# Kernel tuning notes

Hardware: AMD Instinct MI355X
Metric: run time of the kernel (lower is better)

Reference implementation:

```python
import jax, jax.numpy as jnp
import numpy as np

SEG_NUMS = [1, 2, 4, 8, 16, 32, 64, 128, 256, 512]
L = SEG_NUMS[-1]
B, C, VOCAB = 32, 64, 8192
BETA = 0.25
RESI = 0.5  # quant_resi_ratio
N_PHI = 4
# PhiPartiallyShared ticks for K==4: linspace(1/(3K), 1-1/(3K), K)
PHI_TICKS = np.linspace(1.0 / (3 * N_PHI), 1.0 - 1.0 / (3 * N_PHI), N_PHI)


def interp_area(x, size):
    """torch F.interpolate(mode='area') for [B,C,l] when sizes divide evenly."""
    b, c, l = x.shape
    if size == l:
        return x
    if size < l:  # adaptive avg pool == block mean (l % size == 0)
        return x.reshape(b, c, size, l // size).mean(axis=-1)
    return jnp.repeat(x, size // l, axis=-1)  # area upsample == repeat


def phi_apply(h, w, b):
    """Phi: h*(1-r) + Conv1d(h)*r, same padding, ks=3. h:[B,C,l] w:[C,C,3] b:[C]."""
    y = jax.lax.conv_general_dilated(h, w, window_strides=(1,), padding=[(1, 1)],
                                     dimension_numbers=('NCH', 'OIH', 'NCH'))
    y = y + b[None, :, None]
    return h * (1.0 - RESI) + y * RESI


def _normalize(x, axis):
    return x / jnp.maximum(jnp.linalg.norm(x, axis=axis, keepdims=True), 1e-12)


def _mse(a, b):
    return jnp.mean((a - b) ** 2)


def setup_inputs() -> dict:
    key = jax.random.key(0)
    k1, k2, k3 = jax.random.split(key, 3)
    f_BCl = jax.random.normal(k1, (B, C, L), jnp.float32)
    embed_w = jax.random.normal(k2, (VOCAB, C), jnp.float32)
    phi_w = jax.random.normal(k3, (N_PHI, C, C, 3), jnp.float32) * 0.05  # conv-init scale
    phi_b = jnp.zeros((N_PHI, C), jnp.float32)
    return {"f_BCl": f_BCl, "embed_w": embed_w, "phi_w": phi_w, "phi_b": phi_b}


def vq_forward(f, embed_w, phi_w, phi_b):
    f = f.astype(jnp.float32)
    f_ng = jax.lax.stop_gradient(f)
    f_rest = f_ng
    f_hat = jnp.zeros_like(f_ng)
    loss = jnp.asarray(0.0, jnp.float32)
    # argmax uses .data (stop-grad) normalized codebook columns
    cb_n = _normalize(jax.lax.stop_gradient(embed_w), axis=1)  # [V, C]
    num_scales = len(SEG_NUMS)
    for si, s in enumerate(SEG_NUMS):
        rest = interp_area(f_rest, s)                      # [B, C, s] (identity at last scale)
        rest_NC = _normalize(rest.transpose(0, 2, 1).reshape(-1, C), axis=1)  # [B*s, C]
        idx = jnp.argmax(rest_NC @ cb_n.T, axis=1)         # [B*s] cosine-sim lookup
        h = embed_w[idx].reshape(B, s, C).transpose(0, 2, 1)  # gather (differentiable) -> [B,C,s]
        h = interp_area(h, L)
        pidx = int(np.argmin(np.abs(PHI_TICKS - si / (num_scales - 1))))
        h = phi_apply(h, phi_w[pidx], phi_b[pidx])
        f_hat = f_hat + h
        f_rest = f_rest - h
        loss = loss + BETA * _mse(jax.lax.stop_gradient(f_hat), f) + _mse(f_hat, f_ng)
    loss = loss / num_scales
    f_hat_out = jax.lax.stop_gradient(f_hat) - f_ng + f  # straight-through
    return f_hat_out, loss


def reference(f_BCl, embed_w, phi_w, phi_b):
    return vq_forward(f_BCl, embed_w, phi_w, phi_b)
```

## Files before the change

kernel.cpp:

```cpp
#include <hip/hip_runtime.h>


#define B_ 32
#define C_ 64
#define L_ 512
#define V_ 8192

typedef _Float16 half8 __attribute__((ext_vector_type(8)));
typedef float f32x4 __attribute__((ext_vector_type(4)));

#define C11 4.8828125e-4f

__device__ __forceinline__ unsigned enc_f(float s) {
  unsigned u = __float_as_uint(s);
  return (u & 0x80000000u) ? ~u : (u | 0x80000000u);
}

__device__ __forceinline__ void split2(float x, _Float16& h, _Float16& m) {
  h = (_Float16)x;
  float r1 = x - (float)h;
  m = (_Float16)(r1 * 2048.0f);
}

__global__ __launch_bounds__(256) void k_setup(
    const float* __restrict__ f, const float* __restrict__ embed,
    const float* __restrict__ phiw, _Float16* __restrict__ ch,
    _Float16* __restrict__ cm, float* __restrict__ restAll,
    float* __restrict__ lossac, unsigned long long* __restrict__ packed,
    float* __restrict__ phiwT) {
  const int blk = blockIdx.x;
  const int tid = threadIdx.x;
  if (blk < 128) {
    int g = blk * 256 + tid;
    int v = g >> 2;
    int sub = g & 3;
    const float* row = embed + v * 64 + sub * 16;
    float x[16];
    float ss = 0.f;
#pragma unroll
    for (int i = 0; i < 16; i += 4) {
      float4 t = *(const float4*)(row + i);
      x[i] = t.x; x[i + 1] = t.y; x[i + 2] = t.z; x[i + 3] = t.w;
      ss += t.x * t.x + t.y * t.y + t.z * t.z + t.w * t.w;
    }
    ss += __shfl_xor(ss, 1);
    ss += __shfl_xor(ss, 2);
    float rinv = 1.0f / fmaxf(sqrtf(ss), 1e-12f);
    _Float16 hb[16], mb[16];
#pragma unroll
    for (int i = 0; i < 16; i++) split2(x[i] * rinv, hb[i], mb[i]);
    const int kc = sub >> 1;
    const int q0 = (2 * sub) & 3;
    const int q1 = (2 * sub + 1) & 3;
    const int m = v & 15;
    const int blkbase = ((v >> 4) * 2 + kc) * 512;
    *(half8*)(ch + blkbase + (q0 * 16 + m) * 8) = *(half8*)(hb);
    *(half8*)(ch + blkbase + (q1 * 16 + m) * 8) = *(half8*)(hb + 8);
    *(half8*)(cm + blkbase + (q0 * 16 + m) * 8) = *(half8*)(mb);
    *(half8*)(cm + blkbase + (q1 * 16 + m) * 8) = *(half8*)(mb + 8);
  } else if (blk < 640) {
    int sb = blk - 128;
    int b = sb >> 4;
    int c = (sb & 15) * 4 + (tid >> 6);
    int lane = tid & 63;
    const float* row = f + (b * 64 + c) * 512 + lane * 8;
    float4 x0 = *(const float4*)row;
    float4 x1 = *(const float4*)(row + 4);
    float ssum = ((x0.x + x0.y) + (x0.z + x0.w)) +
                 ((x1.x + x1.y) + (x1.z + x1.w));
#pragma unroll
    for (int off = 32; off > 0; off >>= 1) ssum += __shfl_down(ssum, off);
    if (lane == 0) restAll[c * 32 + b] = ssum;
  } else {
    int zg = (blk - 640) * 256 + tid;
    const int ZS = 512 * 256;
    for (int i = zg; i < 126976; i += ZS) restAll[2048 + i] = 0.0f;
    for (int i = zg; i < 32736; i += ZS) packed[i] = 0ull;
    if (zg < 5120) lossac[zg] = 0.0f;
    if (phiwT) {
      for (int i = zg; i < 49152; i += ZS) {
        float v = phiw[i];
        int p = i / 12288;
        int r = i - p * 12288;
        int o = r / 192;
        int r2 = r - o * 192;
        int c = r2 / 3;
        int t = r2 - c * 3;
        phiwT[((p * 3 + t) * 64 + c) * 64 + o] = v;
      }
    }
  }
}

#define ARG_LOAD(BH0, BH1, BM0, BM1, TT)                                   \
  {                                                                        \
    const _Float16* p1 = ch + (code_start + (TT)) * 64 + lane * 8;         \
    const _Float16* p2 = cm + (code_start + (TT)) * 64 + lane * 8;         \
    BH0 = *(const half8*)(p1);                                             \
    BH1 = *(const half8*)(p1 + 512);                                       \
    BM0 = *(const half8*)(p2);                                             \
    BM1 = *(const half8*)(p2 + 512);                                       \
  }

#define ARG_TILE(BH0, BH1, BM0, BM1, TT)                                   \
  {                                                                        \
    const int cid = cs_g + (TT) + m;                                       \
    _Pragma("unroll") for (int mt = 0; mt < MT; mt++) {                    \
      f32x4 a0, a1;                                                        \
      a0 = __builtin_amdgcn_mfma_f32_16x16x32_f16(ah[mt][0], BH0, Z, 0, 0, 0); \
      a1 = __builtin_amdgcn_mfma_f32_16x16x32_f16(ah[mt][0], BM0, Z, 0, 0, 0); \
      a1 = __builtin_amdgcn_mfma_f32_16x16x32_f16(am[mt][0], BH0, a1, 0, 0, 0); \
      a0 = __builtin_amdgcn_mfma_f32_16x16x32_f16(ah[mt][1], BH1, a0, 0, 0, 0); \
      a1 = __builtin_amdgcn_mfma_f32_16x16x32_f16(ah[mt][1], BM1, a1, 0, 0, 0); \
      a1 = __builtin_amdgcn_mfma_f32_16x16x32_f16(am[mt][1], BH1, a1, 0, 0, 0); \
      _Pragma("unroll") for (int r = 0; r < 4; r++) {                      \
        float sc = fmaf(C11, a1[r], a0[r]);                                \
        if (sc > best[mt][r]) { best[mt][r] = sc; bidx[mt][r] = cid; }     \
      }                                                                    \
    }                                                                      \
  }

template <int MT>
__global__ __launch_bounds__(256, 2) void k_argmax3(
    const _Float16* __restrict__ ch, const _Float16* __restrict__ cm,
    const float* __restrict__ restq, unsigned long long* __restrict__ packedq,
    int Q, int mgroups, int wave_codes, int cbase) {
  const int mg = blockIdx.x % mgroups;
  const int sp = blockIdx.x / mgroups;
  const int lane = threadIdx.x & 63;
  const int wave = threadIdx.x >> 6;
  const int qbase = mg * (MT * 16);
  __shared__ _Float16 qh[MT * 16][72];
  __shared__ _Float16 qm[MT * 16][72];
  __shared__ unsigned long long spart[4][MT * 16];
  for (int i = threadIdx.x; i < MT * 16 * 64; i += 256) {
    int c = i / (MT * 16);
    int qq = i % (MT * 16);
    float v = restq[c * Q + qbase + qq];
    _Float16 h, m;
    split2(v, h, m);
    qh[qq][c] = h;
    qm[qq][c] = m;
  }
  __syncthreads();

  const int m = lane & 15;
  const int quad = lane >> 4;
  half8 ah[MT][2], am[MT][2];
#pragma unroll
  for (int mt = 0; mt < MT; mt++)
#pragma unroll
    for (int kc = 0; kc < 2; kc++) {
      ah[mt][kc] = *(const half8*)(&qh[mt * 16 + m][kc * 32 + quad * 8]);
      am[mt][kc] = *(const half8*)(&qm[mt * 16 + m][kc * 32 + quad * 8]);
    }

  float best[MT][4];
  int bidx[MT][4];
#pragma unroll
  for (int mt = 0; mt < MT; mt++)
#pragma unroll
    for (int r = 0; r < 4; r++) { best[mt][r] = -3.4e38f; bidx[mt][r] = 0; }

  const int code_start = (sp * 4 + wave) * wave_codes;
  const int cs_g = cbase + code_start;
  const f32x4 Z = {0.f, 0.f, 0.f, 0.f};

  half8 Ah0, Ah1, Am0, Am1, Bh0, Bh1, Bm0, Bm1;
  ARG_LOAD(Ah0, Ah1, Am0, Am1, 0);
  if (16 < wave_codes) ARG_LOAD(Bh0, Bh1, Bm0, Bm1, 16);
  for (int t = 0; t < wave_codes; t += 32) {
    ARG_TILE(Ah0, Ah1, Am0, Am1, t);
    if (t + 32 < wave_codes) ARG_LOAD(Ah0, Ah1, Am0, Am1, t + 32);
    if (t + 16 < wave_codes) {
      ARG_TILE(Bh0, Bh1, Bm0, Bm1, t + 16);
      if (t + 48 < wave_codes) ARG_LOAD(Bh0, Bh1, Bm0, Bm1, t + 48);
    }
  }

#pragma unroll
  for (int off = 1; off < 16; off <<= 1) {
#pragma unroll
    for (int mt = 0; mt < MT; mt++)
#pragma unroll
      for (int r = 0; r < 4; r++) {
        float ob = __shfl_xor(best[mt][r], off);
        int oi = __shfl_xor(bidx[mt][r], off);
        if (ob > best[mt][r] || (ob == best[mt][r] && oi < bidx[mt][r])) {
          best[mt][r] = ob; bidx[mt][r] = oi;
        }
      }
  }
  if (m == 0) {
#pragma unroll
    for (int mt = 0; mt < MT; mt++)
#pragma unroll
      for (int r = 0; r < 4; r++) {
        unsigned long long pk =
            ((unsigned long long)enc_f(best[mt][r]) << 32) |
            (unsigned)(~bidx[mt][r]);
        spart[wave][mt * 16 + quad * 4 + r] = pk;
      }
  }
  __syncthreads();
  if (threadIdx.x < MT * 16) {
    unsigned long long v = spart[0][threadIdx.x];
    unsigned long long v1 = spart[1][threadIdx.x];
    unsigned long long v2 = spart[2][threadIdx.x];
    unsigned long long v3 = spart[3][threadIdx.x];
    if (v1 > v) v = v1;
    if (v2 > v) v = v2;
    if (v3 > v) v = v3;
    atomicMax(&packedq[qbase + threadIdx.x], v);
  }
}

__global__ __launch_bounds__(256) void k_fused(
    const float* __restrict__ f, const float* __restrict__ embed,
    const float* __restrict__ phiw, const float* __restrict__ phib,
    const float* __restrict__ wT, const unsigned long long* __restrict__ packedq,
    float* __restrict__ restn, float* __restrict__ fhat,
    float* __restrict__ lossac, int s, int log2blk, int pidx, int si,
    int log2blkn) {
  const int ch0 = blockIdx.x * 32;
  const int bb = blockIdx.y;
  const int tid = threadIdx.x;
  const int blkw = 1 << log2blk;
  int j_lo = (ch0 >> log2blk) - 1;
  if (j_lo < 0) j_lo = 0;
  int j_hi = ((ch0 + 31) >> log2blk) + 1;
  if (j_hi > s - 1) j_hi = s - 1;
  const int nseg = j_hi - j_lo + 1;

  __shared__ float hl[34][64];
  __shared__ float abc_l[34][192];

  for (int i = tid; i < nseg * 64; i += 256) {
    int seg = i >> 6, c = i & 63;
    int idx = (int)(~(unsigned)(packedq[bb * s + j_lo + seg]));
    hl[seg][c] = embed[idx * 64 + c];
  }
  __syncthreads();

  {
    const int o = tid & 63;
    const int w4 = tid >> 6;
    const float* wrow = phiw + (pidx * 64 + o) * 192;
    const float* wtp = wT ? (wT + pidx * 12288 + o) : nullptr;
    float acc[9][3];
#pragma unroll
    for (int a = 0; a < 9; a++) { acc[a][0] = acc[a][1] = acc[a][2] = 0.f; }
#pragma unroll
    for (int c4b = 0; c4b < 4; c4b++) {
      float w48[48];
      if (wT) {
        const float* wp = wtp + c4b * 16 * 64;
#pragma unroll
        for (int cc = 0; cc < 16; cc++)
#pragma unroll
          for (int k = 0; k < 3; k++)
            w48[cc * 3 + k] = wp[(k * 64 + cc) * 64];
      } else {
#pragma unroll
        for (int k = 0; k < 12; k++)
          *(float4*)(w48 + 4 * k) = *(const float4*)(wrow + c4b * 48 + 4 * k);
      }
#pragma unroll
      for (int sx = 0; sx < 9; sx++) {
        int seg = w4 + sx * 4;
        if (seg < nseg) {
#pragma unroll
          for (int cc4 = 0; cc4 < 4; cc4++) {
            float4 h4 = *(const float4*)(&hl[seg][c4b * 16 + cc4 * 4]);
            const float hv[4] = {h4.x, h4.y, h4.z, h4.w};
#pragma unroll
            for (int u = 0; u < 4; u++) {
              int cc = cc4 * 4 + u;
              acc[sx][0] = fmaf(w48[cc * 3 + 0], hv[u], acc[sx][0]);
              acc[sx][1] = fmaf(w48[cc * 3 + 1], hv[u], acc[sx][1]);
              acc[sx][2] = fmaf(w48[cc * 3 + 2], hv[u], acc[sx][2]);
            }
          }
        }
      }
    }
#pragma unroll
    for (int sx = 0; sx < 9; sx++) {
      int seg = w4 + sx * 4;
      if (seg < nseg) {
        abc_l[seg][o] = acc[sx][0];
        abc_l[seg][64 + o] = acc[sx][1];
        abc_l[seg][128 + o] = acc[sx][2];
      }
    }
  }
  __syncthreads();

  const int c = tid >> 2;
  const int l0 = ch0 + (tid & 3) * 8;
  const float bias = phib[pidx * 64 + c];
  const int fi0 = (bb * 64 + c) * 512 + l0;
  const float4 fa = *(const float4*)(f + fi0);
  const float4 fb2 = *(const float4*)(f + fi0 + 4);
  float fv[8] = {fa.x, fa.y, fa.z, fa.w, fb2.x, fb2.y, fb2.z, fb2.w};
  float fhv[8] = {0.f, 0.f, 0.f, 0.f, 0.f, 0.f, 0.f, 0.f};
  if (si != 0) {
    const float4 ga = *(const float4*)(fhat + fi0);
    const float4 gb2 = *(const float4*)(fhat + fi0 + 4);
    fhv[0] = ga.x; fhv[1] = ga.y; fhv[2] = ga.z; fhv[3] = ga.w;
    fhv[4] = gb2.x; fhv[5] = gb2.y; fhv[6] = gb2.z; fhv[7] = gb2.w;
  }
  float dv[8];
  float sq = 0.f;
#pragma unroll
  for (int k = 0; k < 8; k++) {
    int l = l0 + k;
    int j = l >> log2blk;
    int jrel = j - j_lo;
    int pos = l & (blkw - 1);
    float y = abc_l[jrel][64 + c] + bias;
    if (pos == 0) {
      if (j > 0) y += abc_l[jrel - 1][c];
    } else {
      y += abc_l[jrel][c];
    }
    if (pos == blkw - 1) {
      if (j < s - 1) y += abc_l[jrel + 1][128 + c];
    } else {
      y += abc_l[jrel][128 + c];
    }
    float ho = 0.5f * (hl[jrel][c] + y);
    float fh = fhv[k] + ho;
    fhv[k] = fh;
    float d = fh - fv[k];
    dv[k] = d;
    sq = fmaf(d, d, sq);
  }
  *(float4*)(fhat + fi0) = make_float4(fhv[0], fhv[1], fhv[2], fhv[3]);
  *(float4*)(fhat + fi0 + 4) = make_float4(fhv[4], fhv[5], fhv[6], fhv[7]);

  if (log2blkn >= 0) {
    const int sn = 512 >> log2blkn;
    const int blkn = 1 << log2blkn;
    const int qb = c * (32 * sn) + bb * sn;
    float rs8 = -(((dv[0] + dv[1]) + (dv[2] + dv[3])) +
                  ((dv[4] + dv[5]) + (dv[6] + dv[7])));
    if (blkn >= 64) {
      float r = rs8;
      r += __shfl_down(r, 2);
      r += __shfl_down(r, 1);
      if ((tid & 3) == 0) atomicAdd(&restn[qb + (l0 >> log2blkn)], r);
    } else if (blkn == 32) {
      float r = rs8;
      r += __shfl_down(r, 2);
      r += __shfl_down(r, 1);
      if ((tid & 3) == 0) restn[qb + (l0 >> 5)] = r;
    } else if (blkn == 16) {
      float r = rs8;
      r += __shfl_down(r, 1);
      if ((tid & 1) == 0) restn[qb + (l0 >> 4)] = r;
    } else if (blkn == 8) {
      restn[qb + (l0 >> 3)] = rs8;
    } else {
      for (int base = 0; base < 8; base += blkn) {
        float rs = 0.f;
        for (int k = 0; k < blkn; k++) rs += dv[base + k];
        restn[qb + ((l0 + base) >> log2blkn)] = -rs;
      }
    }
  }

#pragma unroll
  for (int off = 32; off > 0; off >>= 1) sq += __shfl_down(sq, off);
  __shared__ float red[4];
  const int lane = tid & 63, wave = tid >> 6;
  if (lane == 0) red[wave] = sq;
  __syncthreads();
  if (tid == 0)
    lossac[si * 512 + bb * 16 + blockIdx.x] =
        (red[0] + red[1]) + (red[2] + red[3]);
}

__global__ __launch_bounds__(256) void k_loss(const float* __restrict__ lossac,
                                              float* __restrict__ out) {
  const int tid = threadIdx.x;
  float sum = 0.f;
  for (int i = tid; i < 5120; i += 256) sum += lossac[i];
#pragma unroll
  for (int off = 32; off > 0; off >>= 1) sum += __shfl_down(sum, off);
  __shared__ float red[4];
  if ((tid & 63) == 0) red[tid >> 6] = sum;
  __syncthreads();
  if (tid == 0)
    out[B_ * C_ * L_] = ((red[0] + red[1]) + (red[2] + red[3])) *
                        (1.25f / (10.0f * (float)(B_ * C_ * L_)));
}

extern "C" void kernel_launch(void* const* d_in, const int* in_sizes, int n_in,
                              void* d_out, int out_size, void* d_ws,
                              size_t ws_size, hipStream_t stream) {
  const float* f     = (const float*)d_in[0];
  const float* embed = (const float*)d_in[1];
  const float* phiw  = (const float*)d_in[2];
  const float* phib  = (const float*)d_in[3];
  float* fhat = (float*)d_out;

  _Float16* ch = (_Float16*)d_ws;
  _Float16* cm = ch + V_ * 64;
  float* restAll = (float*)(cm + V_ * 64);
  float* lossac = restAll + 2048 * 1023;
  unsigned long long* packed = (unsigned long long*)(lossac + 5120);
  float* phiwT = (float*)(packed + 32736);
  const size_t WS_NEED = (size_t)((char*)(phiwT + 49152) - (char*)d_ws);
  if (ws_size < WS_NEED) phiwT = nullptr;

  static const int PIDX[10] = {0, 0, 1, 1, 1, 2, 2, 3, 3, 3};
  static const int NSPL[10] = {16, 16, 16, 16, 16, 16, 16, 16, 8, 4};

  k_setup<<<dim3(1152), dim3(256), 0, stream>>>(f, embed, phiw, ch, cm,
                                                restAll, lossac, packed,
                                                phiwT);

  for (int si = 0; si < 10; si++) {
    const int s = 1 << si;
    const int Q = 32 * s;
    const int log2blk = 9 - si;
    const int nsplit = NSPL[si];
    const int wave_codes = V_ / nsplit / 4;
    const float* restq = restAll + 2048 * (s - 1);
    unsigned long long* pq = packed + 32 * (s - 1);

    if (Q >= 64) {
      const int mgroups = Q / 64;
      k_argmax3<4><<<dim3(mgroups * nsplit), dim3(256), 0, stream>>>(
          ch, cm, restq, pq, Q, mgroups, wave_codes, 0);
    } else {
      k_argmax3<2><<<dim3(nsplit), dim3(256), 0, stream>>>(
          ch, cm, restq, pq, Q, 1, wave_codes, 0);
    }

    float* restn = (si < 9) ? (restAll + 2048 * (2 * s - 1)) : nullptr;
    const int log2blkn = (si < 9) ? (8 - si) : -1;
    k_fused<<<dim3(16, 32), dim3(256), 0, stream>>>(
        f, embed, phiw, phib, phiwT, pq, restn, fhat, lossac, s, log2blk,
        PIDX[si], si, log2blkn);
  }
  k_loss<<<dim3(1), dim3(256), 0, stream>>>(lossac, fhat);
}
```

Before: 516.7 us.

## Fuse all stages into one persistent kernel with software grid barriers

Replaces the setup kernel, the twenty per-scale argmax/fused launches and the loss kernel with a single persistent 512-block kernel. Stages are separated by an atomic-counter grid barrier with flag polling, and shared memory is reused through a union. The aim is to remove launch overhead and inter-kernel gaps across about 22 small launches. In exchange, all 512 blocks must be co-resident or the barrier deadlocks, and barrier latency plus idle blocks in the small argmax stages add cost. The phiwT fallback for an undersized workspace is also dropped.

```diff
diff --git a/kernel.cpp b/kernel.cpp
--- a/kernel.cpp
+++ b/kernel.cpp
@@ -5,11 +5,25 @@
 #define C_ 64
 #define L_ 512
 #define V_ 8192
+#define NBLK 512
 
 typedef _Float16 half8 __attribute__((ext_vector_type(8)));
 typedef float f32x4 __attribute__((ext_vector_type(4)));
 
 #define C11 4.8828125e-4f
+
+union SMem {
+  struct {
+    _Float16 qh[64][72];
+    _Float16 qm[64][72];
+    unsigned long long spart[4][64];
+  } am;
+  struct {
+    float hl[34][64];
+    float abc[34][192];
+    float red[4];
+  } fu;
+};
 
 __device__ __forceinline__ unsigned enc_f(float s) {
   unsigned u = __float_as_uint(s);
@@ -22,13 +36,33 @@
   m = (_Float16)(r1 * 2048.0f);
 }
 
-__global__ __launch_bounds__(256) void k_setup(
-    const float* __restrict__ f, const float* __restrict__ embed,
-    const float* __restrict__ phiw, _Float16* __restrict__ ch,
-    _Float16* __restrict__ cm, float* __restrict__ restAll,
-    float* __restrict__ lossac, unsigned long long* __restrict__ packed,
-    float* __restrict__ phiwT) {
-  const int blk = blockIdx.x;
+__device__ __forceinline__ void gbar(unsigned long long* gb, unsigned bar) {
+  __syncthreads();
+  if (threadIdx.x == 0) {
+    __threadfence();
+    unsigned long long old = atomicAdd(gb, 1ull);
+    if (old == (unsigned long long)bar * NBLK - 1ull) {
+#pragma unroll
+      for (int i = 0; i < 8; i++)
+        atomicExch(gb + 32 + i * 32, (unsigned long long)bar);
+    } else {
+      unsigned long long* myf = gb + 32 + (blockIdx.x & 7) * 32;
+      while (atomicAdd(myf, 0ull) < (unsigned long long)bar)
+        __builtin_amdgcn_s_sleep(16);
+    }
+    __threadfence();
+  }
+  __syncthreads();
+}
+
+__device__ void d_setup(int blk, const float* __restrict__ f,
+                        const float* __restrict__ embed,
+                        const float* __restrict__ phiw,
+                        _Float16* __restrict__ ch, _Float16* __restrict__ cm,
+                        float* __restrict__ restAll,
+                        float* __restrict__ lossac,
+                        unsigned long long* __restrict__ packed,
+                        float* __restrict__ phiwT) {
   const int tid = threadIdx.x;
   if (blk < 128) {
     int g = blk * 256 + tid;
@@ -77,17 +111,15 @@
     for (int i = zg; i < 126976; i += ZS) restAll[2048 + i] = 0.0f;
     for (int i = zg; i < 32736; i += ZS) packed[i] = 0ull;
     if (zg < 5120) lossac[zg] = 0.0f;
-    if (phiwT) {
-      for (int i = zg; i < 49152; i += ZS) {
-        float v = phiw[i];
-        int p = i / 12288;
-        int r = i - p * 12288;
-        int o = r / 192;
-        int r2 = r - o * 192;
-        int c = r2 / 3;
-        int t = r2 - c * 3;
-        phiwT[((p * 3 + t) * 64 + c) * 64 + o] = v;
-      }
+    for (int i = zg; i < 49152; i += ZS) {
+      float v = phiw[i];
+      int p = i / 12288;
+      int r = i - p * 12288;
+      int o = r / 192;
+      int r2 = r - o * 192;
+      int c = r2 / 3;
+      int t = r2 - c * 3;
+      phiwT[((p * 3 + t) * 64 + c) * 64 + o] = v;
     }
   }
 }
@@ -104,15 +136,15 @@
 
 #define ARG_TILE(BH0, BH1, BM0, BM1, TT)                                   \
   {                                                                        \
-    const int cid = cs_g + (TT) + m;                                       \
+    const int cid = code_start + (TT) + m;                                 \
     _Pragma("unroll") for (int mt = 0; mt < MT; mt++) {                    \
       f32x4 a0, a1;                                                        \
-      a0 = __builtin_amdgcn_mfma_f32_16x16x32_f16(ah[mt][0], BH0, Z, 0, 0, 0); \
-      a1 = __builtin_amdgcn_mfma_f32_16x16x32_f16(ah[mt][0], BM0, Z, 0, 0, 0); \
-      a1 = __builtin_amdgcn_mfma_f32_16x16x32_f16(am[mt][0], BH0, a1, 0, 0, 0); \
-      a0 = __builtin_amdgcn_mfma_f32_16x16x32_f16(ah[mt][1], BH1, a0, 0, 0, 0); \
-      a1 = __builtin_amdgcn_mfma_f32_16x16x32_f16(ah[mt][1], BM1, a1, 0, 0, 0); \
-      a1 = __builtin_amdgcn_mfma_f32_16x16x32_f16(am[mt][1], BH1, a1, 0, 0, 0); \
+      a0 = __builtin_amdgcn_mfma_f32_16x16x32_f16(ahf[mt][0], BH0, Z, 0, 0, 0); \
+      a1 = __builtin_amdgcn_mfma_f32_16x16x32_f16(ahf[mt][0], BM0, Z, 0, 0, 0); \
+      a1 = __builtin_amdgcn_mfma_f32_16x16x32_f16(amf[mt][0], BH0, a1, 0, 0, 0); \
+      a0 = __builtin_amdgcn_mfma_f32_16x16x32_f16(ahf[mt][1], BH1, a0, 0, 0, 0); \
+      a1 = __builtin_amdgcn_mfma_f32_16x16x32_f16(ahf[mt][1], BM1, a1, 0, 0, 0); \
+      a1 = __builtin_amdgcn_mfma_f32_16x16x32_f16(amf[mt][1], BH1, a1, 0, 0, 0); \
       _Pragma("unroll") for (int r = 0; r < 4; r++) {                      \
         float sc = fmaf(C11, a1[r], a0[r]);                                \
         if (sc > best[mt][r]) { best[mt][r] = sc; bidx[mt][r] = cid; }     \
@@ -121,38 +153,37 @@
   }
 
 template <int MT>
-__global__ __launch_bounds__(256, 2) void k_argmax3(
-    const _Float16* __restrict__ ch, const _Float16* __restrict__ cm,
-    const float* __restrict__ restq, unsigned long long* __restrict__ packedq,
-    int Q, int mgroups, int wave_codes, int cbase) {
+__device__ void d_argmax(SMem* sm, const _Float16* __restrict__ ch,
+                         const _Float16* __restrict__ cm,
+                         const float* __restrict__ restq,
+                         unsigned long long* __restrict__ packedq, int Q,
+                         int mgroups, int nsplit, int wave_codes) {
   const int mg = blockIdx.x % mgroups;
-  const int sp = blockIdx.x / mgroups;
+  const int sp0 = blockIdx.x / mgroups;
+  if (sp0 >= nsplit) return;
   const int lane = threadIdx.x & 63;
   const int wave = threadIdx.x >> 6;
   const int qbase = mg * (MT * 16);
-  __shared__ _Float16 qh[MT * 16][72];
-  __shared__ _Float16 qm[MT * 16][72];
-  __shared__ unsigned long long spart[4][MT * 16];
   for (int i = threadIdx.x; i < MT * 16 * 64; i += 256) {
     int c = i / (MT * 16);
     int qq = i % (MT * 16);
     float v = restq[c * Q + qbase + qq];
     _Float16 h, m;
     split2(v, h, m);
-    qh[qq][c] = h;
-    qm[qq][c] = m;
+    sm->am.qh[qq][c] = h;
+    sm->am.qm[qq][c] = m;
   }
   __syncthreads();
 
   const int m = lane & 15;
   const int quad = lane >> 4;
-  half8 ah[MT][2], am[MT][2];
+  half8 ahf[MT][2], amf[MT][2];
 #pragma unroll
   for (int mt = 0; mt < MT; mt++)
 #pragma unroll
     for (int kc = 0; kc < 2; kc++) {
-      ah[mt][kc] = *(const half8*)(&qh[mt * 16 + m][kc * 32 + quad * 8]);
-      am[mt][kc] = *(const half8*)(&qm[mt * 16 + m][kc * 32 + quad * 8]);
+      ahf[mt][kc] = *(const half8*)(&sm->am.qh[mt * 16 + m][kc * 32 + quad * 8]);
+      amf[mt][kc] = *(const half8*)(&sm->am.qm[mt * 16 + m][kc * 32 + quad * 8]);
     }
 
   float best[MT][4];
@@ -162,19 +193,21 @@
 #pragma unroll
     for (int r = 0; r < 4; r++) { best[mt][r] = -3.4e38f; bidx[mt][r] = 0; }
 
-  const int code_start = (sp * 4 + wave) * wave_codes;
-  const int cs_g = cbase + code_start;
   const f32x4 Z = {0.f, 0.f, 0.f, 0.f};
-
-  half8 Ah0, Ah1, Am0, Am1, Bh0, Bh1, Bm0, Bm1;
-  ARG_LOAD(Ah0, Ah1, Am0, Am1, 0);
-  if (16 < wave_codes) ARG_LOAD(Bh0, Bh1, Bm0, Bm1, 16);
-  for (int t = 0; t < wave_codes; t += 32) {
-    ARG_TILE(Ah0, Ah1, Am0, Am1, t);
-    if (t + 32 < wave_codes) ARG_LOAD(Ah0, Ah1, Am0, Am1, t + 32);
-    if (t + 16 < wave_codes) {
-      ARG_TILE(Bh0, Bh1, Bm0, Bm1, t + 16);
-      if (t + 48 < wave_codes) ARG_LOAD(Bh0, Bh1, Bm0, Bm1, t + 48);
+  const int spstride = NBLK / mgroups;
+
+  for (int sp = sp0; sp < nsplit; sp += spstride) {
+    const int code_start = (sp * 4 + wave) * wave_codes;
+    half8 Ah0, Ah1, Am0, Am1, Bh0, Bh1, Bm0, Bm1;
+    ARG_LOAD(Ah0, Ah1, Am0, Am1, 0);
+    if (16 < wave_codes) ARG_LOAD(Bh0, Bh1, Bm0, Bm1, 16);
+    for (int t = 0; t < wave_codes; t += 32) {
+      ARG_TILE(Ah0, Ah1, Am0, Am1, t);
+      if (t + 32 < wave_codes) ARG_LOAD(Ah0, Ah1, Am0, Am1, t + 32);
+      if (t + 16 < wave_codes) {
+        ARG_TILE(Bh0, Bh1, Bm0, Bm1, t + 16);
+        if (t + 48 < wave_codes) ARG_LOAD(Bh0, Bh1, Bm0, Bm1, t + 48);
+      }
     }
   }
 
@@ -199,15 +232,15 @@
         unsigned long long pk =
             ((unsigned long long)enc_f(best[mt][r]) << 32) |
             (unsigned)(~bidx[mt][r]);
-        spart[wave][mt * 16 + quad * 4 + r] = pk;
+        sm->am.spart[wave][mt * 16 + quad * 4 + r] = pk;
       }
   }
   __syncthreads();
   if (threadIdx.x < MT * 16) {
-    unsigned long long v = spart[0][threadIdx.x];
-    unsigned long long v1 = spart[1][threadIdx.x];
-    unsigned long long v2 = spart[2][threadIdx.x];
-    unsigned long long v3 = spart[3][threadIdx.x];
+    unsigned long long v = sm->am.spart[0][threadIdx.x];
+    unsigned long long v1 = sm->am.spart[1][threadIdx.x];
+    unsigned long long v2 = sm->am.spart[2][threadIdx.x];
+    unsigned long long v3 = sm->am.spart[3][threadIdx.x];
     if (v1 > v) v = v1;
     if (v2 > v) v = v2;
     if (v3 > v) v = v3;
@@ -215,15 +248,16 @@
   }
 }
 
-__global__ __launch_bounds__(256) void k_fused(
-    const float* __restrict__ f, const float* __restrict__ embed,
-    const float* __restrict__ phiw, const float* __restrict__ phib,
-    const float* __restrict__ wT, const unsigned long long* __restrict__ packedq,
-    float* __restrict__ restn, float* __restrict__ fhat,
-    float* __restrict__ lossac, int s, int log2blk, int pidx, int si,
-    int log2blkn) {
-  const int ch0 = blockIdx.x * 32;
-  const int bb = blockIdx.y;
+__device__ void d_fused(SMem* sm, const float* __restrict__ f,
+                        const float* __restrict__ embed,
+                        const float* __restrict__ phib,
+                        const float* __restrict__ wT,
+                        const unsigned long long* __restrict__ packedq,
+                        float* __restrict__ restn, float* __restrict__ fhat,
+                        float* __restrict__ lossac, int s, int log2blk,
+                        int pidx, int si, int log2blkn) {
+  const int ch0 = (blockIdx.x & 15) * 32;
+  const int bb = blockIdx.x >> 4;
   const int tid = threadIdx.x;
   const int blkw = 1 << log2blk;
   int j_lo = (ch0 >> log2blk) - 1;
@@ -232,46 +266,36 @@
   if (j_hi > s - 1) j_hi = s - 1;
   const int nseg = j_hi - j_lo + 1;
 
-  __shared__ float hl[34][64];
-  __shared__ float abc_l[34][192];
-
   for (int i = tid; i < nseg * 64; i += 256) {
     int seg = i >> 6, c = i & 63;
     int idx = (int)(~(unsigned)(packedq[bb * s + j_lo + seg]));
-    hl[seg][c] = embed[idx * 64 + c];
+    sm->fu.hl[seg][c] = embed[idx * 64 + c];
   }
   __syncthreads();
 
   {
     const int o = tid & 63;
     const int w4 = tid >> 6;
-    const float* wrow = phiw + (pidx * 64 + o) * 192;
-    const float* wtp = wT ? (wT + pidx * 12288 + o) : nullptr;
+    const float* wtp = wT + pidx * 12288 + o;
     float acc[9][3];
 #pragma unroll
     for (int a = 0; a < 9; a++) { acc[a][0] = acc[a][1] = acc[a][2] = 0.f; }
 #pragma unroll
     for (int c4b = 0; c4b < 4; c4b++) {
       float w48[48];
-      if (wT) {
-        const float* wp = wtp + c4b * 16 * 64;
-#pragma unroll
-        for (int cc = 0; cc < 16; cc++)
-#pragma unroll
-          for (int k = 0; k < 3; k++)
-            w48[cc * 3 + k] = wp[(k * 64 + cc) * 64];
-      } else {
-#pragma unroll
-        for (int k = 0; k < 12; k++)
-          *(float4*)(w48 + 4 * k) = *(const float4*)(wrow + c4b * 48 + 4 * k);
-      }
+      const float* wp = wtp + c4b * 16 * 64;
+#pragma unroll
+      for (int cc = 0; cc < 16; cc++)
+#pragma unroll
+        for (int k = 0; k < 3; k++)
+          w48[cc * 3 + k] = wp[(k * 64 + cc) * 64];
 #pragma unroll
       for (int sx = 0; sx < 9; sx++) {
         int seg = w4 + sx * 4;
         if (seg < nseg) {
 #pragma unroll
           for (int cc4 = 0; cc4 < 4; cc4++) {
-            float4 h4 = *(const float4*)(&hl[seg][c4b * 16 + cc4 * 4]);
+            float4 h4 = *(const float4*)(&sm->fu.hl[seg][c4b * 16 + cc4 * 4]);
             const float hv[4] = {h4.x, h4.y, h4.z, h4.w};
 #pragma unroll
             for (int u = 0; u < 4; u++) {
@@ -288,9 +312,9 @@
     for (int sx = 0; sx < 9; sx++) {
       int seg = w4 + sx * 4;
       if (seg < nseg) {
-        abc_l[seg][o] = acc[sx][0];
-        abc_l[seg][64 + o] = acc[sx][1];
-        abc_l[seg][128 + o] = acc[sx][2];
+        sm->fu.abc[seg][o] = acc[sx][0];
+        sm->fu.abc[seg][64 + o] = acc[sx][1];
+        sm->fu.abc[seg][128 + o] = acc[sx][2];
       }
     }
   }
@@ -318,18 +342,18 @@
     int j = l >> log2blk;
     int jrel = j - j_lo;
     int pos = l & (blkw - 1);
-    float y = abc_l[jrel][64 + c] + bias;
+    float y = sm->fu.abc[jrel][64 + c] + bias;
     if (pos == 0) {
-      if (j > 0) y += abc_l[jrel - 1][c];
+      if (j > 0) y += sm->fu.abc[jrel - 1][c];
     } else {
-      y += abc_l[jrel][c];
+      y += sm->fu.abc[jrel][c];
     }
     if (pos == blkw - 1) {
-      if (j < s - 1) y += abc_l[jrel + 1][128 + c];
+      if (j < s - 1) y += sm->fu.abc[jrel + 1][128 + c];
     } else {
-      y += abc_l[jrel][128 + c];
-    }
-    float ho = 0.5f * (hl[jrel][c] + y);
+      y += sm->fu.abc[jrel][128 + c];
+    }
+    float ho = 0.5f * (sm->fu.hl[jrel][c] + y);
     float fh = fhv[k] + ho;
     fhv[k] = fh;
     float d = fh - fv[k];
@@ -372,28 +396,65 @@
 
 #pragma unroll
   for (int off = 32; off > 0; off >>= 1) sq += __shfl_down(sq, off);
-  __shared__ float red[4];
   const int lane = tid & 63, wave = tid >> 6;
-  if (lane == 0) red[wave] = sq;
+  if (lane == 0) sm->fu.red[wave] = sq;
   __syncthreads();
   if (tid == 0)
-    lossac[si * 512 + bb * 16 + blockIdx.x] =
-        (red[0] + red[1]) + (red[2] + red[3]);
-}
-
-__global__ __launch_bounds__(256) void k_loss(const float* __restrict__ lossac,
-                                              float* __restrict__ out) {
+    lossac[si * 512 + blockIdx.x] =
+        (sm->fu.red[0] + sm->fu.red[1]) + (sm->fu.red[2] + sm->fu.red[3]);
+}
+
+__device__ void d_loss(SMem* sm, const float* __restrict__ lossac,
+                       float* __restrict__ out) {
   const int tid = threadIdx.x;
   float sum = 0.f;
   for (int i = tid; i < 5120; i += 256) sum += lossac[i];
 #pragma unroll
   for (int off = 32; off > 0; off >>= 1) sum += __shfl_down(sum, off);
-  __shared__ float red[4];
-  if ((tid & 63) == 0) red[tid >> 6] = sum;
+  if ((tid & 63) == 0) sm->fu.red[tid >> 6] = sum;
   __syncthreads();
   if (tid == 0)
-    out[B_ * C_ * L_] = ((red[0] + red[1]) + (red[2] + red[3])) *
+    out[B_ * C_ * L_] = ((sm->fu.red[0] + sm->fu.red[1]) +
+                         (sm->fu.red[2] + sm->fu.red[3])) *
                         (1.25f / (10.0f * (float)(B_ * C_ * L_)));
+}
+
+__global__ __launch_bounds__(256, 2) void k_mega(
+    const float* __restrict__ f, const float* __restrict__ embed,
+    const float* __restrict__ phiw, const float* __restrict__ phib,
+    _Float16* __restrict__ ch, _Float16* __restrict__ cm,
+    float* __restrict__ restAll, float* __restrict__ lossac,
+    unsigned long long* __restrict__ packed, float* __restrict__ phiwT,
+    unsigned long long* __restrict__ gb, float* __restrict__ fhat) {
+  __shared__ SMem sm;
+  unsigned bar = 0;
+
+  for (int vb = blockIdx.x; vb < 1152; vb += NBLK)
+    d_setup(vb, f, embed, phiw, ch, cm, restAll, lossac, packed, phiwT);
+  gbar(gb, ++bar);
+
+  for (int si = 0; si < 10; si++) {
+    const int s = 1 << si;
+    const int Q = 32 * s;
+    const int nsplit = (si <= 7) ? 16 : ((si == 8) ? 8 : 4);
+    const int wave_codes = V_ / nsplit / 4;
+    const int pidx = (si >= 7) ? 3 : ((si >= 5) ? 2 : ((si >= 2) ? 1 : 0));
+    const float* restq = restAll + 2048 * (s - 1);
+    unsigned long long* pq = packed + 32 * (s - 1);
+
+    if (Q >= 64)
+      d_argmax<4>(&sm, ch, cm, restq, pq, Q, Q / 64, nsplit, wave_codes);
+    else
+      d_argmax<2>(&sm, ch, cm, restq, pq, Q, 1, nsplit, wave_codes);
+    gbar(gb, ++bar);
+
+    float* restn = (si < 9) ? (restAll + 2048 * (2 * s - 1)) : nullptr;
+    d_fused(&sm, f, embed, phib, phiwT, pq, restn, fhat, lossac, s, 9 - si,
+            pidx, si, (si < 9) ? (8 - si) : -1);
+    gbar(gb, ++bar);
+  }
+
+  if (blockIdx.x == 0) d_loss(&sm, lossac, fhat);
 }
 
 extern "C" void kernel_launch(void* const* d_in, const int* in_sizes, int n_in,
@@ -411,39 +472,11 @@
   float* lossac = restAll + 2048 * 1023;
   unsigned long long* packed = (unsigned long long*)(lossac + 5120);
   float* phiwT = (float*)(packed + 32736);
-  const size_t WS_NEED = (size_t)((char*)(phiwT + 49152) - (char*)d_ws);
-  if (ws_size < WS_NEED) phiwT = nullptr;
-
-  static const int PIDX[10] = {0, 0, 1, 1, 1, 2, 2, 3, 3, 3};
-  static const int NSPL[10] = {16, 16, 16, 16, 16, 16, 16, 16, 8, 4};
-
-  k_setup<<<dim3(1152), dim3(256), 0, stream>>>(f, embed, phiw, ch, cm,
-                                                restAll, lossac, packed,
-                                                phiwT);
-
-  for (int si = 0; si < 10; si++) {
-    const int s = 1 << si;
-    const int Q = 32 * s;
-    const int log2blk = 9 - si;
-    const int nsplit = NSPL[si];
-    const int wave_codes = V_ / nsplit / 4;
-    const float* restq = restAll + 2048 * (s - 1);
-    unsigned long long* pq = packed + 32 * (s - 1);
-
-    if (Q >= 64) {
-      const int mgroups = Q / 64;
-      k_argmax3<4><<<dim3(mgroups * nsplit), dim3(256), 0, stream>>>(
-          ch, cm, restq, pq, Q, mgroups, wave_codes, 0);
-    } else {
-      k_argmax3<2><<<dim3(nsplit), dim3(256), 0, stream>>>(
-          ch, cm, restq, pq, Q, 1, wave_codes, 0);
-    }
-
-    float* restn = (si < 9) ? (restAll + 2048 * (2 * s - 1)) : nullptr;
-    const int log2blkn = (si < 9) ? (8 - si) : -1;
-    k_fused<<<dim3(16, 32), dim3(256), 0, stream>>>(
-        f, embed, phiw, phib, phiwT, pq, restn, fhat, lossac, s, log2blk,
-        PIDX[si], si, log2blkn);
-  }
-  k_loss<<<dim3(1), dim3(256), 0, stream>>>(lossac, fhat);
-}
+  unsigned long long* gbarmem = (unsigned long long*)(phiwT + 49152);
+
+  hipMemsetAsync(gbarmem, 0, 320 * sizeof(unsigned long long), stream);
+
+  k_mega<<<dim3(NBLK), dim3(256), 0, stream>>>(
+      f, embed, phiw, phib, ch, cm, restAll, lossac, packed, phiwT, gbarmem,
+      fhat);
+}
```

New measurement: 767.9 us. 1.49x slower.
